# Kernel tuning notes

Measured on AMD Instinct MI355X. Metric: run time of the kernel, lower is better.

Reference implementation:

```python
import jax, jax.numpy as jnp
import numpy as np

DIM = 768
HEADS = 12
HEAD_DIM = DIM // HEADS


def setup_inputs() -> dict:
    key = jax.random.key(0)
    ks = jax.random.split(key, 6)
    B, Nq, Nkv = 2, 2048, 2048
    s = 0.02
    return {
        "query_source": jax.random.normal(ks[0], (B, Nq, DIM), jnp.float32),
        "kv_source": jax.random.normal(ks[1], (B, Nkv, DIM), jnp.float32),
        "Wq": jax.random.normal(ks[2], (DIM, DIM), jnp.float32) * s,
        "Wkv": jax.random.normal(ks[3], (DIM, 2 * DIM), jnp.float32) * s,
        "Wproj": jax.random.normal(ks[4], (DIM, DIM), jnp.float32) * s,
        "bproj": jax.random.normal(ks[5], (DIM,), jnp.float32) * s,
    }


def reference(query_source, kv_source, Wq, Wkv, Wproj, bproj):
    B, Nq, D = query_source.shape
    Nkv = kv_source.shape[1]
    scale = HEAD_DIM ** -0.5
    # projections (qkv_bias=False)
    q = (query_source @ Wq).reshape(B, Nq, HEADS, HEAD_DIM)
    kv = (kv_source @ Wkv).reshape(B, Nkv, 2, HEADS, HEAD_DIM)
    k, v = kv[:, :, 0], kv[:, :, 1]  # (B, Nkv, H, Dh)
    # scores: (B, H, Nq, Nkv)
    attn = jnp.einsum("bqhd,bkhd->bhqk", q, k) * scale
    attn = jax.nn.softmax(attn, axis=-1)
    # attn_drop = 0 (eval)
    x = jnp.einsum("bhqk,bkhd->bqhd", attn, v).reshape(B, Nq, D)
    return x @ Wproj + bproj
```

## Files before the change

kernel.cpp:

```cpp
#include <hip/hip_runtime.h>
#include <math.h>
#include <stdint.h>

typedef __bf16 bf16_t;
typedef __attribute__((ext_vector_type(8))) __bf16 bf16x8;
typedef __attribute__((ext_vector_type(4))) __bf16 bf16x4;
typedef __attribute__((ext_vector_type(4))) float f32x4;

#define DIM   768
#define HEADS 12
#define HD    64
#define NB    2
#define NQ    2048
#define NKV   2048
#define MROWS 4096
#define NQKV  2304

__device__ __forceinline__ float fast_exp2(float x)
{
#if __has_builtin(__builtin_amdgcn_exp2f)
    return __builtin_amdgcn_exp2f(x);
#else
    return exp2f(x);
#endif
}

__device__ __forceinline__ uint32_t pack_bf16x2(float a, float b)
{
    const uint32_t lo = __builtin_bit_cast(uint32_t, a) + 0x8000u;
    const uint32_t hi = __builtin_bit_cast(uint32_t, b) + 0x8000u;
#if __has_builtin(__builtin_amdgcn_perm)
    return __builtin_amdgcn_perm(hi, lo, 0x07060302u);
#else
    return (lo >> 16) | (hi & 0xffff0000u);
#endif
}

__device__ __forceinline__ void async_copy16(const bf16_t* g, bf16_t* l)
{
    typedef const __attribute__((address_space(1))) uint32_t* gp_t;
    typedef __attribute__((address_space(3))) uint32_t* lp_t;
    __builtin_amdgcn_global_load_lds((gp_t)(const void*)g, (lp_t)(void*)l, 16, 0, 0);
}

__global__ void prep_kernel(const float* __restrict__ qs, bf16_t* __restrict__ qs_bf,
                            const float* __restrict__ kvs, bf16_t* __restrict__ kvs_bf,
                            const float* __restrict__ Wq, const float* __restrict__ Wkv,
                            const float* __restrict__ Wproj, bf16_t* __restrict__ Wt,
                            float escale)
{
    __shared__ float tile[32][33];
    const int z = blockIdx.z;
    if (z < 2) {
        const float* in  = z ? kvs : qs;
        bf16_t*      out = z ? kvs_bf : qs_bf;
        const int i = (blockIdx.x * 256 + threadIdx.x) * 8;
        bf16x8 v;
#pragma unroll
        for (int j = 0; j < 8; j++) v[j] = (bf16_t)in[i + j];
        *(bf16x8*)(out + i) = v;
        return;
    }
    const int N   = (z == 3) ? 2 * DIM : DIM;
    const int nb  = N / 32;
    const int idx = blockIdx.x;
    if (idx >= nb * (DIM / 32)) return;
    const float* W = (z == 2) ? Wq : (z == 3) ? Wkv : Wproj;
    bf16_t* T = Wt + ((z == 2) ? (size_t)0 : (z == 3) ? (size_t)DIM * DIM
                                                      : (size_t)NQKV * DIM);
    const float scl = (z == 2) ? escale : 1.0f;
    const int n0 = (idx % nb) * 32, k0 = (idx / nb) * 32;
    const int tx = threadIdx.x & 31, ty = threadIdx.x >> 5;
#pragma unroll
    for (int i = 0; i < 4; i++)
        tile[ty + i * 8][tx] = W[(size_t)(k0 + ty + i * 8) * N + n0 + tx];
    __syncthreads();
#pragma unroll
    for (int i = 0; i < 4; i++)
        T[(size_t)(n0 + ty + i * 8) * DIM + k0 + tx] = (bf16_t)(tile[tx][ty + i * 8] * scl);
}

template<int MODE, int TN>
__global__ __launch_bounds__(256)
void gemm_bk64(const bf16_t* __restrict__ Aq, const bf16_t* __restrict__ Akv,
               const bf16_t* __restrict__ Bt,
               bf16_t* __restrict__ Qb, bf16_t* __restrict__ Kb, bf16_t* __restrict__ Vtb,
               float* __restrict__ ofp, const float* __restrict__ bias)
{
    constexpr int K  = DIM;
    constexpr int NT = TN / 32;
    constexpr int ABLK = 128 * 64;
    constexpr int BBLK = TN * 64;
    constexpr int STEP = ABLK + BBLK;
    constexpr int TRELEMS = (MODE == 0) ? 128 * 136 : 0;
    constexpr int SELEMS = (2 * STEP > TRELEMS) ? 2 * STEP : TRELEMS;
    __shared__ __align__(16) bf16_t smem[SELEMS];

    const int tid  = threadIdx.x;
    const int wave = tid >> 6, lane = tid & 63;
    const int quad = lane >> 4, l16 = lane & 15, l7 = l16 & 7;
    const int bm = blockIdx.x * 128, bn = blockIdx.y * TN;
    const int wm = (wave >> 1) * 64, wn = (wave & 1) * (TN / 2);

    const bf16_t* A = (MODE == 0) ? (bn < DIM ? Aq : Akv) : Aq;

    const int srow = tid >> 3;
    const int scol = ((tid & 7) ^ (srow & 7)) * 8;
    const bf16_t* Ag[4];
    const bf16_t* Bg[NT];
#pragma unroll
    for (int i = 0; i < 4; i++)
        Ag[i] = A + (size_t)(bm + i * 32 + srow) * K + scol;
#pragma unroll
    for (int i = 0; i < NT; i++)
        Bg[i] = Bt + (size_t)(bn + i * 32 + srow) * K + scol;

    f32x4 acc[4][NT] = {};

    {
        bf16_t* AsL = smem + tid * 8;
        bf16_t* BsL = smem + ABLK + tid * 8;
#pragma unroll
        for (int i = 0; i < 4; i++) async_copy16(Ag[i], AsL + i * 2048);
#pragma unroll
        for (int i = 0; i < NT; i++) async_copy16(Bg[i], BsL + i * 2048);
    }
    __syncthreads();

    for (int t = 0; t < K / 64; t++) {
        bf16_t* Ac = smem + (t & 1) * STEP;
        bf16_t* Bc = Ac + ABLK;

        if (t + 1 < K / 64) {
            bf16_t* AsL = smem + ((t + 1) & 1) * STEP + tid * 8;
            bf16_t* BsL = AsL + ABLK;
            const int k1 = (t + 1) * 64;
#pragma unroll
            for (int i = 0; i < 4; i++) async_copy16(Ag[i] + k1, AsL + i * 2048);
#pragma unroll
            for (int i = 0; i < NT; i++) async_copy16(Bg[i] + k1, BsL + i * 2048);
        }

#pragma unroll
        for (int ks = 0; ks < 2; ks++) {
            const int pc = ((ks * 4 + quad) ^ l7) * 8;
            bf16x8 af[4], bfr[NT];
#pragma unroll
            for (int mt = 0; mt < 4; mt++)
                af[mt] = *(const bf16x8*)(&Ac[(wm + mt * 16 + l16) * 64 + pc]);
#pragma unroll
            for (int nt = 0; nt < NT; nt++)
                bfr[nt] = *(const bf16x8*)(&Bc[(wn + nt * 16 + l16) * 64 + pc]);
#pragma unroll
            for (int mt = 0; mt < 4; mt++)
#pragma unroll
                for (int nt = 0; nt < NT; nt++)
                    acc[mt][nt] = __builtin_amdgcn_mfma_f32_16x16x32_bf16(
                        af[mt], bfr[nt], acc[mt][nt], 0, 0, 0);
        }

        __syncthreads();
    }

    if (MODE == 1) {
#pragma unroll
        for (int mt = 0; mt < 4; mt++)
#pragma unroll
            for (int nt = 0; nt < NT; nt++)
#pragma unroll
                for (int r = 0; r < 4; r++) {
                    const int gm = bm + wm + mt * 16 + quad * 4 + r;
                    const int gn = bn + wn + nt * 16 + l16;
                    ofp[(size_t)gm * DIM + gn] = acc[mt][nt][r] + bias[gn];
                }
    } else if (bn < DIM) {
#pragma unroll
        for (int mt = 0; mt < 4; mt++)
#pragma unroll
            for (int nt = 0; nt < NT; nt++)
#pragma unroll
                for (int r = 0; r < 4; r++) {
                    const int gm = bm + wm + mt * 16 + quad * 4 + r;
                    const int gn = bn + wn + nt * 16 + l16;
                    Qb[(size_t)gm * DIM + gn] = (bf16_t)acc[mt][nt][r];
                }
    } else if (bn < 2 * DIM) {
#pragma unroll
        for (int mt = 0; mt < 4; mt++)
#pragma unroll
            for (int nt = 0; nt < NT; nt++)
#pragma unroll
                for (int r = 0; r < 4; r++) {
                    const int gm = bm + wm + mt * 16 + quad * 4 + r;
                    const int gn = bn + wn + nt * 16 + l16 - DIM;
                    Kb[(size_t)gm * DIM + gn] = (bf16_t)acc[mt][nt][r];
                }
    } else {
        bf16_t* tr = smem;
#pragma unroll
        for (int mt = 0; mt < 4; mt++)
#pragma unroll
            for (int nt = 0; nt < NT; nt++) {
                bf16x4 tv;
#pragma unroll
                for (int r = 0; r < 4; r++) tv[r] = (bf16_t)acc[mt][nt][r];
                *(bf16x4*)(&tr[(wn + nt * 16 + l16) * 136 + wm + mt * 16 + quad * 4]) = tv;
            }
        __syncthreads();
        const int b = bm >> 11, kv0 = bm & 2047;
        const int n2base = bn - 2 * DIM;
        const int cg = tid & 15, cc = cg >> 2, cq = cg & 3;
#pragma unroll
        for (int i = 0; i < TN / 16; i++) {
            const int row = i * 16 + (tid >> 4);
            const int n2 = n2base + row, h = n2 >> 6, d = n2 & 63;
            const bf16x4 lo4 = *(const bf16x4*)(&tr[row * 136 + cc * 32 + cq * 4]);
            const bf16x4 hi4 = *(const bf16x4*)(&tr[row * 136 + cc * 32 + 16 + cq * 4]);
            bf16x8 vv;
#pragma unroll
            for (int j = 0; j < 4; j++) { vv[j] = lo4[j]; vv[4 + j] = hi4[j]; }
            *(bf16x8*)(Vtb + ((size_t)(b * HEADS + h) * HD + d) * NKV + kv0 + cg * 8) = vv;
        }
    }
}

__global__ __launch_bounds__(256, 4)
void attn_kernel(const bf16_t* __restrict__ Qb, const bf16_t* __restrict__ Kb,
                 const bf16_t* __restrict__ Vt, bf16_t* __restrict__ Xb)
{
    __shared__ __align__(16) bf16_t kvbuf[16384];
    __shared__ float libuf[4][2][16];

    const int tid  = threadIdx.x;
    const int wave = tid >> 6, lane = tid & 63;
    const int quad = lane >> 4, l16 = lane & 15;
    const int l7   = l16 & 7;
    const int qh = wave & 1, kvh = wave >> 1;

    const int id   = blockIdx.x + (NB * HEADS) * blockIdx.y;
    const int xcd  = id & 7, slot = id >> 3;
    const int bh   = xcd + 8 * (slot >> 5);
    const int b = bh / HEADS, h = bh % HEADS;
    const int q0 = (slot & 31) * 64;

    const bf16_t* Qp = Qb + (size_t)b * NQ * DIM + h * HD;
    const bf16_t* Kp = Kb + (size_t)b * NKV * DIM + h * HD;
    const bf16_t* Vp = Vt + (size_t)(b * HEADS + h) * HD * NKV;

    bf16x8 qf[2][2];
#pragma unroll
    for (int qt = 0; qt < 2; qt++)
#pragma unroll
        for (int ks = 0; ks < 2; ks++)
            qf[qt][ks] = *(const bf16x8*)(Qp + (size_t)(q0 + qh * 32 + qt * 16 + l16) * DIM
                                          + ks * 32 + quad * 8);

    const int kl8 = lane >> 3;
    const bf16_t* Kg0 = Kp + (size_t)(wave * 32 + kl8) * DIM + (((lane & 7) ^ kl8) * 8);
    const int vl4 = lane >> 4, vp = lane & 15;
    const bf16_t* Vg0[4];
#pragma unroll
    for (int i = 0; i < 4; i++) {
        const int d = wave * 16 + i * 4 + vl4;
        const int c = (vp & 8) | ((vp & 7) ^ (d & 7));
        Vg0[i] = Vp + (size_t)d * NKV + c * 8;
    }
    bf16_t* KgL = kvbuf + wave * 2048 + lane * 8;
    bf16_t* VgL = kvbuf + 8192 + wave * 2048 + lane * 8;

    f32x4 o[4][2] = {};
    float li[2] = {0.0f, 0.0f};

    for (int t = 0; t < NKV / 128; t++) {
        const int kv0 = t * 128;
#pragma unroll
        for (int i = 0; i < 4; i++)
            async_copy16(Kg0 + (size_t)(kv0 + i * 8) * DIM, KgL + i * 512);
#pragma unroll
        for (int i = 0; i < 4; i++)
            async_copy16(Vg0[i] + kv0, VgL + i * 512);
        __syncthreads();

        f32x4 s[4][2] = {};
        __builtin_amdgcn_s_setprio(1);
#pragma unroll
        for (int kt = 0; kt < 4; kt++)
#pragma unroll
            for (int ks = 0; ks < 2; ks++) {
                const bf16x8 kf = *(const bf16x8*)(&kvbuf[
                    (kvh * 64 + kt * 16 + l16) * 64 + ((((ks << 2) | quad) ^ l7) * 8)]);
#pragma unroll
                for (int qt = 0; qt < 2; qt++)
                    s[kt][qt] = __builtin_amdgcn_mfma_f32_16x16x32_bf16(
                        kf, qf[qt][ks], s[kt][qt], 0, 0, 0);
            }
        __builtin_amdgcn_s_setprio(0);

        bf16x8 pb[2][2];
#pragma unroll
        for (int qt = 0; qt < 2; qt++) {
            float p[16];
#pragma unroll
            for (int kt = 0; kt < 4; kt++)
#pragma unroll
                for (int r = 0; r < 4; r++) p[kt * 4 + r] = fast_exp2(s[kt][qt][r]);
            float rs = 0.0f;
#pragma unroll
            for (int j = 0; j < 16; j++) rs += p[j];
            li[qt] += rs;
#pragma unroll
            for (int kc = 0; kc < 2; kc++) {
                union { uint32_t u[4]; bf16x8 v; } pu;
#pragma unroll
                for (int i = 0; i < 4; i++)
                    pu.u[i] = pack_bf16x2(p[kc * 8 + 2 * i], p[kc * 8 + 2 * i + 1]);
                pb[qt][kc] = pu.v;
            }
        }

        __builtin_amdgcn_s_setprio(1);
#pragma unroll
        for (int dt = 0; dt < 4; dt++) {
            const int droff = 8192 + (dt * 16 + l16) * 128;
#pragma unroll
            for (int kc = 0; kc < 2; kc++) {
                const bf16x8 vf = *(const bf16x8*)(&kvbuf[
                    droff + (kvh * 8 + ((kc * 4 + quad) ^ l7)) * 8]);
#pragma unroll
                for (int qt = 0; qt < 2; qt++)
                    o[dt][qt] = __builtin_amdgcn_mfma_f32_16x16x32_bf16(
                        vf, pb[qt][kc], o[dt][qt], 0, 0, 0);
            }
        }
        __builtin_amdgcn_s_setprio(0);
        __syncthreads();
    }

#pragma unroll
    for (int qt = 0; qt < 2; qt++) {
        li[qt] += __shfl_xor(li[qt], 16);
        li[qt] += __shfl_xor(li[qt], 32);
    }
    if (quad == 0) { libuf[wave][0][l16] = li[0]; libuf[wave][1][l16] = li[1]; }

    float* ob = (float*)(kvbuf + qh * 8192);
    if (kvh == 1) {
#pragma unroll
        for (int dt = 0; dt < 4; dt++)
#pragma unroll
            for (int qt = 0; qt < 2; qt++)
#pragma unroll
                for (int r = 0; r < 4; r++)
                    ob[(dt * 16 + quad * 4 + r) * 33 + qt * 16 + l16] = o[dt][qt][r];
    }
    __syncthreads();
    if (kvh == 0) {
        const float inv0 = 1.0f / (li[0] + libuf[2 + qh][0][l16]);
        const float inv1 = 1.0f / (li[1] + libuf[2 + qh][1][l16]);
#pragma unroll
        for (int dt = 0; dt < 4; dt++)
#pragma unroll
            for (int qt = 0; qt < 2; qt++)
#pragma unroll
                for (int r = 0; r < 4; r++)
                    o[dt][qt][r] = (o[dt][qt][r]
                                    + ob[(dt * 16 + quad * 4 + r) * 33 + qt * 16 + l16])
                                   * (qt ? inv1 : inv0);
    }
    __syncthreads();
    bf16_t* Ob16 = kvbuf;
    if (kvh == 0) {
#pragma unroll
        for (int dt = 0; dt < 4; dt++)
#pragma unroll
            for (int qt = 0; qt < 2; qt++) {
                bf16x4 ov;
#pragma unroll
                for (int r = 0; r < 4; r++) ov[r] = (bf16_t)o[dt][qt][r];
                *(bf16x4*)(&Ob16[(qh * 32 + qt * 16 + l16) * 72 + dt * 16 + quad * 4]) = ov;
            }
    }
    __syncthreads();
    {
        const int row = tid >> 2, ch = (tid & 3) * 16;
        bf16_t* dst = Xb + (size_t)(b * NQ + q0 + row) * DIM + h * HD + ch;
        *(bf16x8*)(dst)     = *(const bf16x8*)(&Ob16[row * 72 + ch]);
        *(bf16x8*)(dst + 8) = *(const bf16x8*)(&Ob16[row * 72 + ch + 8]);
    }
}

extern "C" void kernel_launch(void* const* d_in, const int* in_sizes, int n_in,
                              void* d_out, int out_size, void* d_ws, size_t ws_size,
                              hipStream_t stream)
{
    const float* qs    = (const float*)d_in[0];
    const float* kvs   = (const float*)d_in[1];
    const float* Wq    = (const float*)d_in[2];
    const float* Wkv   = (const float*)d_in[3];
    const float* Wproj = (const float*)d_in[4];
    const float* bproj = (const float*)d_in[5];
    float* out = (float*)d_out;

    bf16_t* w = (bf16_t*)d_ws;
    bf16_t* qs_bf  = w;  w += (size_t)MROWS * DIM;
    bf16_t* kvs_bf = w;  w += (size_t)MROWS * DIM;
    bf16_t* Wt     = w;  w += (size_t)NQKV * DIM;
    bf16_t* Wprojt = w;  w += (size_t)DIM * DIM;
    bf16_t* Qb     = w;  w += (size_t)MROWS * DIM;
    bf16_t* Kb     = w;  w += (size_t)MROWS * DIM;
    bf16_t* Vtb    = w;  w += (size_t)MROWS * DIM;
    bf16_t* Xb     = qs_bf;

    const float escale = 0.125f * 1.44269504088896341f;
    prep_kernel<<<dim3(MROWS * DIM / 2048, 1, 5), 256, 0, stream>>>(
        qs, qs_bf, kvs, kvs_bf, Wq, Wkv, Wproj, Wt, escale);

    gemm_bk64<0, 96><<<dim3(MROWS / 128, NQKV / 96), 256, 0, stream>>>(
        qs_bf, kvs_bf, Wt, Qb, Kb, Vtb, nullptr, nullptr);
    attn_kernel<<<dim3(NB * HEADS, NQ / 64), 256, 0, stream>>>(Qb, Kb, Vtb, Xb);
    gemm_bk64<1, 32><<<dim3(MROWS / 128, DIM / 32), 256, 0, stream>>>(
        Xb, nullptr, Wprojt, nullptr, nullptr, nullptr, out, bproj);
}
```

Measured before the change: 154.3 us.

## Double-buffer K/V tiles and give each wave its own query rows

The attention kernel now loads 64-key K/V tiles into two alternating LDS buffers, prefetching the next tile while the current one is computed. Previously it used a single buffer of 128 keys with two wave pairs splitting the key range. Each wave now owns 16 query rows over the full key range, which removes the end-of-kernel partial-sum exchange and the extra barriers. The aim is to hide global-load latency and cut the reduction cost. In exchange, each K/V fragment read from LDS now feeds one MFMA instead of two, which raises LDS traffic per MFMA.

```diff
diff --git a/kernel.cpp b/kernel.cpp
--- a/kernel.cpp
+++ b/kernel.cpp
@@ -228,14 +228,12 @@
 void attn_kernel(const bf16_t* __restrict__ Qb, const bf16_t* __restrict__ Kb,
                  const bf16_t* __restrict__ Vt, bf16_t* __restrict__ Xb)
 {
-    __shared__ __align__(16) bf16_t kvbuf[16384];
-    __shared__ float libuf[4][2][16];
+    __shared__ __align__(16) bf16_t kvbuf[2][8192];
 
     const int tid  = threadIdx.x;
     const int wave = tid >> 6, lane = tid & 63;
     const int quad = lane >> 4, l16 = lane & 15;
     const int l7   = l16 & 7;
-    const int qh = wave & 1, kvh = wave >> 1;
 
     const int id   = blockIdx.x + (NB * HEADS) * blockIdx.y;
     const int xcd  = id & 7, slot = id >> 3;
@@ -247,138 +245,101 @@
     const bf16_t* Kp = Kb + (size_t)b * NKV * DIM + h * HD;
     const bf16_t* Vp = Vt + (size_t)(b * HEADS + h) * HD * NKV;
 
-    bf16x8 qf[2][2];
-#pragma unroll
-    for (int qt = 0; qt < 2; qt++)
-#pragma unroll
-        for (int ks = 0; ks < 2; ks++)
-            qf[qt][ks] = *(const bf16x8*)(Qp + (size_t)(q0 + qh * 32 + qt * 16 + l16) * DIM
-                                          + ks * 32 + quad * 8);
-
-    const int kl8 = lane >> 3;
-    const bf16_t* Kg0 = Kp + (size_t)(wave * 32 + kl8) * DIM + (((lane & 7) ^ kl8) * 8);
-    const int vl4 = lane >> 4, vp = lane & 15;
-    const bf16_t* Vg0[4];
-#pragma unroll
-    for (int i = 0; i < 4; i++) {
-        const int d = wave * 16 + i * 4 + vl4;
-        const int c = (vp & 8) | ((vp & 7) ^ (d & 7));
-        Vg0[i] = Vp + (size_t)d * NKV + c * 8;
-    }
-    bf16_t* KgL = kvbuf + wave * 2048 + lane * 8;
-    bf16_t* VgL = kvbuf + 8192 + wave * 2048 + lane * 8;
-
-    f32x4 o[4][2] = {};
-    float li[2] = {0.0f, 0.0f};
-
-    for (int t = 0; t < NKV / 128; t++) {
-        const int kv0 = t * 128;
-#pragma unroll
-        for (int i = 0; i < 4; i++)
-            async_copy16(Kg0 + (size_t)(kv0 + i * 8) * DIM, KgL + i * 512);
-#pragma unroll
-        for (int i = 0; i < 4; i++)
-            async_copy16(Vg0[i] + kv0, VgL + i * 512);
-        __syncthreads();
-
-        f32x4 s[4][2] = {};
+    const int sr = tid >> 3, sp = tid & 7;
+    const bf16_t* KgA = Kp + (size_t)sr * DIM + ((sp ^ (sr & 7)) * 8);
+    const bf16_t* VgA = Vp + (size_t)sr * NKV + ((sp ^ (sr & 7)) * 8);
+
+    {
+        bf16_t* kb = kvbuf[0] + tid * 8;
+#pragma unroll
+        for (int i = 0; i < 2; i++)
+            async_copy16(KgA + (size_t)(i * 32) * DIM, kb + i * 2048);
+#pragma unroll
+        for (int i = 0; i < 2; i++)
+            async_copy16(VgA + (size_t)(i * 32) * NKV, kb + 4096 + i * 2048);
+    }
+
+    bf16x8 qf[2];
+#pragma unroll
+    for (int ks = 0; ks < 2; ks++)
+        qf[ks] = *(const bf16x8*)(Qp + (size_t)(q0 + wave * 16 + l16) * DIM
+                                  + ks * 32 + quad * 8);
+
+    f32x4 o[4] = {};
+    float li = 0.0f;
+
+    __syncthreads();
+
+    for (int t = 0; t < NKV / 64; t++) {
+        const bf16_t* kv = kvbuf[t & 1];
+
+        if (t + 1 < NKV / 64) {
+            bf16_t* kb = kvbuf[(t + 1) & 1] + tid * 8;
+            const int kv1 = (t + 1) * 64;
+#pragma unroll
+            for (int i = 0; i < 2; i++)
+                async_copy16(KgA + (size_t)(kv1 + i * 32) * DIM, kb + i * 2048);
+#pragma unroll
+            for (int i = 0; i < 2; i++)
+                async_copy16(VgA + (size_t)(i * 32) * NKV + kv1, kb + 4096 + i * 2048);
+        }
+
+        f32x4 s[4] = {};
         __builtin_amdgcn_s_setprio(1);
 #pragma unroll
         for (int kt = 0; kt < 4; kt++)
 #pragma unroll
             for (int ks = 0; ks < 2; ks++) {
-                const bf16x8 kf = *(const bf16x8*)(&kvbuf[
-                    (kvh * 64 + kt * 16 + l16) * 64 + ((((ks << 2) | quad) ^ l7) * 8)]);
-#pragma unroll
-                for (int qt = 0; qt < 2; qt++)
-                    s[kt][qt] = __builtin_amdgcn_mfma_f32_16x16x32_bf16(
-                        kf, qf[qt][ks], s[kt][qt], 0, 0, 0);
+                const bf16x8 kf = *(const bf16x8*)(&kv[
+                    (kt * 16 + l16) * 64 + (((ks * 4 + quad) ^ l7) * 8)]);
+                s[kt] = __builtin_amdgcn_mfma_f32_16x16x32_bf16(kf, qf[ks], s[kt], 0, 0, 0);
             }
         __builtin_amdgcn_s_setprio(0);
 
-        bf16x8 pb[2][2];
-#pragma unroll
-        for (int qt = 0; qt < 2; qt++) {
-            float p[16];
-#pragma unroll
-            for (int kt = 0; kt < 4; kt++)
-#pragma unroll
-                for (int r = 0; r < 4; r++) p[kt * 4 + r] = fast_exp2(s[kt][qt][r]);
-            float rs = 0.0f;
-#pragma unroll
-            for (int j = 0; j < 16; j++) rs += p[j];
-            li[qt] += rs;
+        float p[16];
+#pragma unroll
+        for (int kt = 0; kt < 4; kt++)
+#pragma unroll
+            for (int r = 0; r < 4; r++) p[kt * 4 + r] = fast_exp2(s[kt][r]);
+        float rs = 0.0f;
+#pragma unroll
+        for (int j = 0; j < 16; j++) rs += p[j];
+        li += rs;
+        bf16x8 pb[2];
+#pragma unroll
+        for (int kc = 0; kc < 2; kc++) {
+            union { uint32_t u[4]; bf16x8 v; } pu;
+#pragma unroll
+            for (int i = 0; i < 4; i++)
+                pu.u[i] = pack_bf16x2(p[kc * 8 + 2 * i], p[kc * 8 + 2 * i + 1]);
+            pb[kc] = pu.v;
+        }
+
+        __builtin_amdgcn_s_setprio(1);
+#pragma unroll
+        for (int dt = 0; dt < 4; dt++)
 #pragma unroll
             for (int kc = 0; kc < 2; kc++) {
-                union { uint32_t u[4]; bf16x8 v; } pu;
-#pragma unroll
-                for (int i = 0; i < 4; i++)
-                    pu.u[i] = pack_bf16x2(p[kc * 8 + 2 * i], p[kc * 8 + 2 * i + 1]);
-                pb[qt][kc] = pu.v;
+                const bf16x8 vf = *(const bf16x8*)(&kv[
+                    4096 + (dt * 16 + l16) * 64 + (((kc * 4 + quad) ^ l7) * 8)]);
+                o[dt] = __builtin_amdgcn_mfma_f32_16x16x32_bf16(vf, pb[kc], o[dt], 0, 0, 0);
             }
-        }
-
-        __builtin_amdgcn_s_setprio(1);
-#pragma unroll
-        for (int dt = 0; dt < 4; dt++) {
-            const int droff = 8192 + (dt * 16 + l16) * 128;
-#pragma unroll
-            for (int kc = 0; kc < 2; kc++) {
-                const bf16x8 vf = *(const bf16x8*)(&kvbuf[
-                    droff + (kvh * 8 + ((kc * 4 + quad) ^ l7)) * 8]);
-#pragma unroll
-                for (int qt = 0; qt < 2; qt++)
-                    o[dt][qt] = __builtin_amdgcn_mfma_f32_16x16x32_bf16(
-                        vf, pb[qt][kc], o[dt][qt], 0, 0, 0);
-            }
-        }
         __builtin_amdgcn_s_setprio(0);
+
         __syncthreads();
     }
 
-#pragma unroll
-    for (int qt = 0; qt < 2; qt++) {
-        li[qt] += __shfl_xor(li[qt], 16);
-        li[qt] += __shfl_xor(li[qt], 32);
-    }
-    if (quad == 0) { libuf[wave][0][l16] = li[0]; libuf[wave][1][l16] = li[1]; }
-
-    float* ob = (float*)(kvbuf + qh * 8192);
-    if (kvh == 1) {
-#pragma unroll
-        for (int dt = 0; dt < 4; dt++)
-#pragma unroll
-            for (int qt = 0; qt < 2; qt++)
-#pragma unroll
-                for (int r = 0; r < 4; r++)
-                    ob[(dt * 16 + quad * 4 + r) * 33 + qt * 16 + l16] = o[dt][qt][r];
-    }
-    __syncthreads();
-    if (kvh == 0) {
-        const float inv0 = 1.0f / (li[0] + libuf[2 + qh][0][l16]);
-        const float inv1 = 1.0f / (li[1] + libuf[2 + qh][1][l16]);
-#pragma unroll
-        for (int dt = 0; dt < 4; dt++)
-#pragma unroll
-            for (int qt = 0; qt < 2; qt++)
-#pragma unroll
-                for (int r = 0; r < 4; r++)
-                    o[dt][qt][r] = (o[dt][qt][r]
-                                    + ob[(dt * 16 + quad * 4 + r) * 33 + qt * 16 + l16])
-                                   * (qt ? inv1 : inv0);
-    }
-    __syncthreads();
-    bf16_t* Ob16 = kvbuf;
-    if (kvh == 0) {
-#pragma unroll
-        for (int dt = 0; dt < 4; dt++)
-#pragma unroll
-            for (int qt = 0; qt < 2; qt++) {
-                bf16x4 ov;
-#pragma unroll
-                for (int r = 0; r < 4; r++) ov[r] = (bf16_t)o[dt][qt][r];
-                *(bf16x4*)(&Ob16[(qh * 32 + qt * 16 + l16) * 72 + dt * 16 + quad * 4]) = ov;
-            }
+    li += __shfl_xor(li, 16);
+    li += __shfl_xor(li, 32);
+    const float inv = 1.0f / li;
+
+    bf16_t* Ob16 = &kvbuf[0][0];
+#pragma unroll
+    for (int dt = 0; dt < 4; dt++) {
+        bf16x4 ov;
+#pragma unroll
+        for (int r = 0; r < 4; r++) ov[r] = (bf16_t)(o[dt][r] * inv);
+        *(bf16x4*)(&Ob16[(wave * 16 + l16) * 72 + dt * 16 + quad * 4]) = ov;
     }
     __syncthreads();
     {
```

Measured after the change: 152.3 us. No clear change (-1.3%).

## Double-buffer KV tiles and split attention KV across all four waves

Applied to the files above, without the earlier changes.

Adds a second LDS K/V buffer and issues the next tile's async loads before computing on the current one, so global-to-LDS transfer overlaps MFMA work instead of stalling at a barrier each iteration. Work is repartitioned so each wave handles all 64 query rows against its own 32-key slice, with a tree reduction of the four partial outputs and row sums at the end. It also replaces the custom bf16 packing with plain casts. LDS usage doubles and occupancy hint drops from 4 to 2 blocks per CU, and the epilogue reduction is longer.

```diff
diff --git a/kernel.cpp b/kernel.cpp
--- a/kernel.cpp
+++ b/kernel.cpp
@@ -22,17 +22,6 @@
     return __builtin_amdgcn_exp2f(x);
 #else
     return exp2f(x);
-#endif
-}
-
-__device__ __forceinline__ uint32_t pack_bf16x2(float a, float b)
-{
-    const uint32_t lo = __builtin_bit_cast(uint32_t, a) + 0x8000u;
-    const uint32_t hi = __builtin_bit_cast(uint32_t, b) + 0x8000u;
-#if __has_builtin(__builtin_amdgcn_perm)
-    return __builtin_amdgcn_perm(hi, lo, 0x07060302u);
-#else
-    return (lo >> 16) | (hi & 0xffff0000u);
 #endif
 }
 
@@ -224,18 +213,17 @@
     }
 }
 
-__global__ __launch_bounds__(256, 4)
+__global__ __launch_bounds__(256, 2)
 void attn_kernel(const bf16_t* __restrict__ Qb, const bf16_t* __restrict__ Kb,
                  const bf16_t* __restrict__ Vt, bf16_t* __restrict__ Xb)
 {
-    __shared__ __align__(16) bf16_t kvbuf[16384];
-    __shared__ float libuf[4][2][16];
+    __shared__ __align__(16) bf16_t kvbuf[2][16384];
+    __shared__ float libuf[4][4][16];
 
     const int tid  = threadIdx.x;
     const int wave = tid >> 6, lane = tid & 63;
     const int quad = lane >> 4, l16 = lane & 15;
     const int l7   = l16 & 7;
-    const int qh = wave & 1, kvh = wave >> 1;
 
     const int id   = blockIdx.x + (NB * HEADS) * blockIdx.y;
     const int xcd  = id & 7, slot = id >> 3;
@@ -247,137 +235,156 @@
     const bf16_t* Kp = Kb + (size_t)b * NKV * DIM + h * HD;
     const bf16_t* Vp = Vt + (size_t)(b * HEADS + h) * HD * NKV;
 
-    bf16x8 qf[2][2];
-#pragma unroll
-    for (int qt = 0; qt < 2; qt++)
+    const int ksr = tid >> 3, ksp = tid & 7;
+    const bf16_t* KgA = Kp + (size_t)ksr * DIM + ((ksp ^ (ksr & 7)) * 8);
+    const int vsd = tid >> 4, vsp = tid & 15;
+    const bf16_t* VgA = Vp + (size_t)vsd * NKV + ((vsp ^ (vsd & 7)) * 8);
+
+    {
+        bf16_t* kb = kvbuf[0] + tid * 8;
+        bf16_t* vb = kvbuf[0] + 8192 + tid * 8;
+#pragma unroll
+        for (int i = 0; i < 4; i++) async_copy16(KgA + (size_t)(i * 32) * DIM, kb + i * 2048);
+#pragma unroll
+        for (int i = 0; i < 4; i++) async_copy16(VgA + (size_t)(i * 16) * NKV, vb + i * 2048);
+    }
+
+    bf16x8 qf[4][2];
+#pragma unroll
+    for (int qt = 0; qt < 4; qt++)
 #pragma unroll
         for (int ks = 0; ks < 2; ks++)
-            qf[qt][ks] = *(const bf16x8*)(Qp + (size_t)(q0 + qh * 32 + qt * 16 + l16) * DIM
+            qf[qt][ks] = *(const bf16x8*)(Qp + (size_t)(q0 + qt * 16 + l16) * DIM
                                           + ks * 32 + quad * 8);
 
-    const int kl8 = lane >> 3;
-    const bf16_t* Kg0 = Kp + (size_t)(wave * 32 + kl8) * DIM + (((lane & 7) ^ kl8) * 8);
-    const int vl4 = lane >> 4, vp = lane & 15;
-    const bf16_t* Vg0[4];
-#pragma unroll
-    for (int i = 0; i < 4; i++) {
-        const int d = wave * 16 + i * 4 + vl4;
-        const int c = (vp & 8) | ((vp & 7) ^ (d & 7));
-        Vg0[i] = Vp + (size_t)d * NKV + c * 8;
-    }
-    bf16_t* KgL = kvbuf + wave * 2048 + lane * 8;
-    bf16_t* VgL = kvbuf + 8192 + wave * 2048 + lane * 8;
-
-    f32x4 o[4][2] = {};
-    float li[2] = {0.0f, 0.0f};
+    f32x4 o[4][4] = {};
+    float li[4] = {0.0f, 0.0f, 0.0f, 0.0f};
+
+    __syncthreads();
 
     for (int t = 0; t < NKV / 128; t++) {
-        const int kv0 = t * 128;
-#pragma unroll
-        for (int i = 0; i < 4; i++)
-            async_copy16(Kg0 + (size_t)(kv0 + i * 8) * DIM, KgL + i * 512);
-#pragma unroll
-        for (int i = 0; i < 4; i++)
-            async_copy16(Vg0[i] + kv0, VgL + i * 512);
-        __syncthreads();
-
-        f32x4 s[4][2] = {};
+        const bf16_t* kv = kvbuf[t & 1];
+
+        if (t + 1 < NKV / 128) {
+            bf16_t* kb = kvbuf[(t + 1) & 1] + tid * 8;
+            bf16_t* vb = kvbuf[(t + 1) & 1] + 8192 + tid * 8;
+            const int kv1 = (t + 1) * 128;
+#pragma unroll
+            for (int i = 0; i < 4; i++)
+                async_copy16(KgA + (size_t)(kv1 + i * 32) * DIM, kb + i * 2048);
+#pragma unroll
+            for (int i = 0; i < 4; i++)
+                async_copy16(VgA + (size_t)(i * 16) * NKV + kv1, vb + i * 2048);
+        }
+
+        f32x4 s[2][4] = {};
         __builtin_amdgcn_s_setprio(1);
 #pragma unroll
-        for (int kt = 0; kt < 4; kt++)
+        for (int kt = 0; kt < 2; kt++)
 #pragma unroll
             for (int ks = 0; ks < 2; ks++) {
-                const bf16x8 kf = *(const bf16x8*)(&kvbuf[
-                    (kvh * 64 + kt * 16 + l16) * 64 + ((((ks << 2) | quad) ^ l7) * 8)]);
-#pragma unroll
-                for (int qt = 0; qt < 2; qt++)
+                const bf16x8 kf = *(const bf16x8*)(&kv[
+                    (wave * 32 + kt * 16 + l16) * 64 + (((ks * 4 + quad) ^ l7) * 8)]);
+#pragma unroll
+                for (int qt = 0; qt < 4; qt++)
                     s[kt][qt] = __builtin_amdgcn_mfma_f32_16x16x32_bf16(
                         kf, qf[qt][ks], s[kt][qt], 0, 0, 0);
             }
         __builtin_amdgcn_s_setprio(0);
 
-        bf16x8 pb[2][2];
-#pragma unroll
-        for (int qt = 0; qt < 2; qt++) {
-            float p[16];
-#pragma unroll
-            for (int kt = 0; kt < 4; kt++)
-#pragma unroll
-                for (int r = 0; r < 4; r++) p[kt * 4 + r] = fast_exp2(s[kt][qt][r]);
+        bf16x8 pb[4];
+#pragma unroll
+        for (int qt = 0; qt < 4; qt++) {
+            float pj[8];
+#pragma unroll
+            for (int kt = 0; kt < 2; kt++)
+#pragma unroll
+                for (int r = 0; r < 4; r++) pj[kt * 4 + r] = fast_exp2(s[kt][qt][r]);
             float rs = 0.0f;
 #pragma unroll
-            for (int j = 0; j < 16; j++) rs += p[j];
+            for (int j = 0; j < 8; j++) rs += pj[j];
             li[qt] += rs;
-#pragma unroll
-            for (int kc = 0; kc < 2; kc++) {
-                union { uint32_t u[4]; bf16x8 v; } pu;
-#pragma unroll
-                for (int i = 0; i < 4; i++)
-                    pu.u[i] = pack_bf16x2(p[kc * 8 + 2 * i], p[kc * 8 + 2 * i + 1]);
-                pb[qt][kc] = pu.v;
-            }
+            bf16x8 t8;
+#pragma unroll
+            for (int j = 0; j < 8; j++) t8[j] = (bf16_t)pj[j];
+            pb[qt] = t8;
         }
 
         __builtin_amdgcn_s_setprio(1);
 #pragma unroll
         for (int dt = 0; dt < 4; dt++) {
-            const int droff = 8192 + (dt * 16 + l16) * 128;
-#pragma unroll
-            for (int kc = 0; kc < 2; kc++) {
-                const bf16x8 vf = *(const bf16x8*)(&kvbuf[
-                    droff + (kvh * 8 + ((kc * 4 + quad) ^ l7)) * 8]);
-#pragma unroll
-                for (int qt = 0; qt < 2; qt++)
-                    o[dt][qt] = __builtin_amdgcn_mfma_f32_16x16x32_bf16(
-                        vf, pb[qt][kc], o[dt][qt], 0, 0, 0);
-            }
+            const bf16x8 vf = *(const bf16x8*)(&kv[
+                8192 + (dt * 16 + l16) * 128 + (((wave * 4 + quad) ^ l7) * 8)]);
+#pragma unroll
+            for (int qt = 0; qt < 4; qt++)
+                o[dt][qt] = __builtin_amdgcn_mfma_f32_16x16x32_bf16(
+                    vf, pb[qt], o[dt][qt], 0, 0, 0);
         }
         __builtin_amdgcn_s_setprio(0);
+
         __syncthreads();
     }
 
 #pragma unroll
-    for (int qt = 0; qt < 2; qt++) {
+    for (int qt = 0; qt < 4; qt++) {
         li[qt] += __shfl_xor(li[qt], 16);
         li[qt] += __shfl_xor(li[qt], 32);
     }
-    if (quad == 0) { libuf[wave][0][l16] = li[0]; libuf[wave][1][l16] = li[1]; }
-
-    float* ob = (float*)(kvbuf + qh * 8192);
-    if (kvh == 1) {
+    if (quad == 0)
+#pragma unroll
+        for (int qt = 0; qt < 4; qt++) libuf[wave][qt][l16] = li[qt];
+
+    float* R = (float*)&kvbuf[0][0];
+    const int rr = quad * 4;
+    if (wave >= 2) {
+        float* Rw = R + (size_t)(wave - 2) * (64 * 66);
 #pragma unroll
         for (int dt = 0; dt < 4; dt++)
 #pragma unroll
-            for (int qt = 0; qt < 2; qt++)
+            for (int qt = 0; qt < 4; qt++)
 #pragma unroll
                 for (int r = 0; r < 4; r++)
-                    ob[(dt * 16 + quad * 4 + r) * 33 + qt * 16 + l16] = o[dt][qt][r];
-    }
-    __syncthreads();
-    if (kvh == 0) {
-        const float inv0 = 1.0f / (li[0] + libuf[2 + qh][0][l16]);
-        const float inv1 = 1.0f / (li[1] + libuf[2 + qh][1][l16]);
+                    Rw[(dt * 16 + rr + r) * 66 + qt * 16 + l16] = o[dt][qt][r];
+    }
+    __syncthreads();
+    if (wave < 2) {
+        float* Rw = R + (size_t)wave * (64 * 66);
 #pragma unroll
         for (int dt = 0; dt < 4; dt++)
 #pragma unroll
-            for (int qt = 0; qt < 2; qt++)
+            for (int qt = 0; qt < 4; qt++)
 #pragma unroll
                 for (int r = 0; r < 4; r++)
-                    o[dt][qt][r] = (o[dt][qt][r]
-                                    + ob[(dt * 16 + quad * 4 + r) * 33 + qt * 16 + l16])
-                                   * (qt ? inv1 : inv0);
-    }
-    __syncthreads();
-    bf16_t* Ob16 = kvbuf;
-    if (kvh == 0) {
+                    o[dt][qt][r] += Rw[(dt * 16 + rr + r) * 66 + qt * 16 + l16];
+    }
+    __syncthreads();
+    if (wave == 1) {
 #pragma unroll
         for (int dt = 0; dt < 4; dt++)
 #pragma unroll
-            for (int qt = 0; qt < 2; qt++) {
+            for (int qt = 0; qt < 4; qt++)
+#pragma unroll
+                for (int r = 0; r < 4; r++)
+                    R[(dt * 16 + rr + r) * 66 + qt * 16 + l16] = o[dt][qt][r];
+    }
+    __syncthreads();
+    bf16_t* Ob16 = (bf16_t*)(R + 2 * 64 * 66);
+    if (wave == 0) {
+        float inv[4];
+#pragma unroll
+        for (int qt = 0; qt < 4; qt++)
+            inv[qt] = 1.0f / (libuf[0][qt][l16] + libuf[1][qt][l16]
+                              + libuf[2][qt][l16] + libuf[3][qt][l16]);
+#pragma unroll
+        for (int dt = 0; dt < 4; dt++)
+#pragma unroll
+            for (int qt = 0; qt < 4; qt++) {
                 bf16x4 ov;
 #pragma unroll
-                for (int r = 0; r < 4; r++) ov[r] = (bf16_t)o[dt][qt][r];
-                *(bf16x4*)(&Ob16[(qh * 32 + qt * 16 + l16) * 72 + dt * 16 + quad * 4]) = ov;
+                for (int r = 0; r < 4; r++)
+                    ov[r] = (bf16_t)((o[dt][qt][r]
+                                      + R[(dt * 16 + rr + r) * 66 + qt * 16 + l16]) * inv[qt]);
+                *(bf16x4*)(&Ob16[(qt * 16 + l16) * 72 + dt * 16 + rr]) = ov;
             }
     }
     __syncthreads();
```

After: 163.5 us. 6.0% more time.
